# Kernel tuning notes

Measured on AMD Instinct MI355X. Metric: run time of the kernel, lower is better.

The kernel has to match this reference:

```python
import jax, jax.numpy as jnp
import numpy as np


def setup_inputs() -> dict:
    key = jax.random.key(0)
    ks = jax.random.split(key, 6)
    B, U, T, E, H = 8, 128, 256, 128, 128
    # Xavier-uniform scale for linear layers
    def xavier(k, shape):
        fan_in, fan_out = shape[0], shape[1]
        lim = jnp.sqrt(6.0 / (fan_in + fan_out))
        return jax.random.uniform(k, shape, jnp.float32, -lim, lim)
    return {
        "ue": jax.random.normal(ks[0], (B, U, E), jnp.float32),
        "te": jax.random.normal(ks[1], (B, T, E), jnp.float32),
        "ge": jax.random.normal(ks[2], (B, E), jnp.float32),
        "W1": xavier(ks[3], (3 * E, H)),
        "b1": jnp.zeros((H,), jnp.float32),
        "W2": xavier(ks[4], (H, H)),
        "b2": jnp.zeros((H,), jnp.float32),
        "W3": xavier(ks[5], (H, 1)),
        "b3": jnp.zeros((1,), jnp.float32),
    }


def reference(ue, te, ge, W1, b1, W2, b2, W3, b3):
    # Equivalent to cat([u,t,g], -1) @ W1: decompose W1 into per-source blocks
    # and broadcast-add, avoiding the [B,U,T,3E] intermediate.
    E = ue.shape[-1]
    W1u, W1t, W1g = W1[:E], W1[E:2 * E], W1[2 * E:]
    h = (jnp.einsum("bue,eh->buh", ue, W1u)[:, :, None, :]
         + jnp.einsum("bte,eh->bth", te, W1t)[:, None, :, :]
         + (ge @ W1g)[:, None, None, :]
         + b1)                                   # [B,U,T,H]
    h = jax.nn.gelu(h, approximate=False)        # torch nn.GELU default = exact erf
    h = jax.nn.gelu(h @ W2 + b2, approximate=False)
    logits = (h @ W3 + b3)[..., 0]               # [B,U,T]
    B, U, T = logits.shape
    return logits.reshape(B, U * T)
```

## Files before the change

kernel.cpp:

```cpp
#include <hip/hip_runtime.h>
#include <hip/hip_bf16.h>
#include <math.h>

#define E_ 128
#define H_ 128
#define B_ 8
#define U_ 128
#define T_ 256

typedef short short8 __attribute__((ext_vector_type(8)));
typedef unsigned short ushortx8 __attribute__((ext_vector_type(8)));
typedef float floatx4 __attribute__((ext_vector_type(4)));

__device__ __forceinline__ unsigned short f2bf(float f) {
    union { __hip_bfloat16 b; unsigned short u; } cv;
    cv.b = __float2bfloat16(f);
    return cv.u;
}
__device__ __forceinline__ float bf2f(unsigned short u) {
    union { unsigned int u; float f; } cv;
    cv.u = ((unsigned int)u) << 16;
    return cv.f;
}

__device__ __forceinline__ int sw(int row, int cblk) {
    return row * 128 + (((cblk ^ (row & 15)) << 3));
}

__device__ __forceinline__ float gelu_fast(float x) {
    float x2 = x * x;
    float p = x * __builtin_fmaf(x2, 0.1029407583f, 2.3022586210f);
    float e = __builtin_amdgcn_exp2f(-p);
    return x * __builtin_amdgcn_rcpf(1.0f + e);
}

__global__ __launch_bounds__(256) void stage1_kernel(
    const float* __restrict__ ue, const float* __restrict__ te,
    const float* __restrict__ ge, const float* __restrict__ W1,
    const float* __restrict__ b1, const float* __restrict__ W2,
    float* __restrict__ hu_ws, unsigned short* __restrict__ ht_bf,
    float* __restrict__ gu_ws, unsigned short* __restrict__ w2t_ws)
{
    const int blk = blockIdx.x;
    const int tid = threadIdx.x;

    if (blk < 24) {
        __shared__ unsigned short a_s[128 * 128];
        __shared__ unsigned short w_s[128 * 128];
        const float* __restrict__ A;
        const float* __restrict__ W;
        const bool is_ue = (blk < 8);
        if (is_ue) { A = ue + (size_t)blk * 128 * E_;       W = W1; }
        else       { A = te + (size_t)(blk - 8) * 128 * E_; W = W1 + E_ * H_; }

        const float4* __restrict__ Av = (const float4*)A;
        #pragma unroll
        for (int i = 0; i < 16; i++) {
            const int v = tid + i * 256;
            const int row = v >> 5, c4 = (v & 31) * 4;
            const float4 f = Av[v];
            ushort4 u4 = make_ushort4(f2bf(f.x), f2bf(f.y), f2bf(f.z), f2bf(f.w));
            *(ushort4*)(&a_s[sw(row, c4 >> 3) + (c4 & 7)]) = u4;
        }
        const float4* __restrict__ Wv = (const float4*)W;
        #pragma unroll
        for (int i = 0; i < 16; i++) {
            const int v = tid + i * 256;
            const int k = v >> 5, n4 = (v & 31) * 4;
            const float4 f = Wv[v];
            const int c = k >> 3, off = k & 7;
            w_s[sw(n4 + 0, c) + off] = f2bf(f.x);
            w_s[sw(n4 + 1, c) + off] = f2bf(f.y);
            w_s[sw(n4 + 2, c) + off] = f2bf(f.z);
            w_s[sw(n4 + 3, c) + off] = f2bf(f.w);
        }
        __syncthreads();

        const int wave = tid >> 6, lane = tid & 63;
        const int quad = lane >> 4, l16 = lane & 15;
        const int r0 = wave * 32 + l16;

        floatx4 acc[2][8];
        #pragma unroll
        for (int m = 0; m < 2; m++)
            #pragma unroll
            for (int nt = 0; nt < 8; nt++) acc[m][nt] = (floatx4){0.f, 0.f, 0.f, 0.f};

        #pragma unroll
        for (int kk = 0; kk < 4; kk++) {
            const int c = kk * 4 + quad;
            short8 af0 = *(const short8*)(&a_s[sw(r0, c)]);
            short8 af1 = *(const short8*)(&a_s[sw(r0 + 16, c)]);
            #pragma unroll
            for (int nt = 0; nt < 8; nt++) {
                short8 bf = *(const short8*)(&w_s[sw(nt * 16 + l16, c)]);
                acc[0][nt] = __builtin_amdgcn_mfma_f32_16x16x32_bf16(af0, bf, acc[0][nt], 0, 0, 0);
                acc[1][nt] = __builtin_amdgcn_mfma_f32_16x16x32_bf16(af1, bf, acc[1][nt], 0, 0, 0);
            }
        }
        if (is_ue) {
            float* __restrict__ outp = hu_ws + (size_t)blk * 128 * H_;
            #pragma unroll
            for (int m = 0; m < 2; m++) {
                const int rowb = wave * 32 + m * 16 + quad * 4;
                #pragma unroll
                for (int nt = 0; nt < 8; nt++) {
                    const int col = nt * 16 + l16;
                    #pragma unroll
                    for (int r = 0; r < 4; r++)
                        outp[(size_t)(rowb + r) * H_ + col] = acc[m][nt][r];
                }
            }
        } else {
            unsigned short* __restrict__ outp = ht_bf + (size_t)(blk - 8) * 128 * H_;
            #pragma unroll
            for (int m = 0; m < 2; m++) {
                const int rowb = wave * 32 + m * 16 + quad * 4;
                #pragma unroll
                for (int nt = 0; nt < 8; nt++) {
                    const int col = nt * 16 + l16;
                    #pragma unroll
                    for (int r = 0; r < 4; r++)
                        outp[(size_t)(rowb + r) * H_ + col] = f2bf(acc[m][nt][r]);
                }
            }
        }
    } else if (blk < 28) {
        __shared__ float ge_s[2][E_];
        const int rbase = (blk - 24) * 2;
        const int half = tid >> 7, n = tid & 127;
        ge_s[half][n] = ge[(rbase + half) * E_ + n];
        __syncthreads();
        const float* __restrict__ W1g = W1 + 2 * E_ * H_;
        float acc = b1[n];
        #pragma unroll 8
        for (int e = 0; e < E_; e++)
            acc = __builtin_fmaf(ge_s[half][e], W1g[e * H_ + n], acc);
        gu_ws[(rbase + half) * H_ + n] = acc;
    } else {
        const int base = (blk - 28) * 2048;
        #pragma unroll
        for (int i = 0; i < 8; i++) {
            const int o = base + tid + i * 256;
            const int n = o >> 7, k = o & 127;
            w2t_ws[o] = f2bf(W2[k * H_ + n]);
        }
    }
}

__global__ __launch_bounds__(256, 2) void stage2_kernel(
    const float* __restrict__ hu_ws, const unsigned short* __restrict__ ht_bf,
    const float* __restrict__ gu_ws,
    const unsigned short* __restrict__ w2t_ws,
    const float* __restrict__ b2, const float* __restrict__ W3,
    const float* __restrict__ b3, float* __restrict__ out)
{
    __shared__ unsigned short w2s[128 * 128];
    __shared__ unsigned short ht_s[128 * 128];
    __shared__ float hu_s[H_];
    __shared__ float b2_s[H_];
    __shared__ float w3_s[H_];

    const int tid = threadIdx.x;
    const int t0 = blockIdx.x * 128;
    const int u  = blockIdx.y;
    const int b  = blockIdx.z;

    #pragma unroll
    for (int i = 0; i < 8; i++) {
        const int v = tid + i * 256;
        const int n = v >> 4, c = v & 15;
        *(ushortx8*)(&w2s[sw(n, c)]) = *(const ushortx8*)(w2t_ws + n * 128 + c * 8);
    }
    const unsigned short* __restrict__ htg = ht_bf + ((size_t)(b * T_ + t0)) * H_;
    #pragma unroll
    for (int i = 0; i < 8; i++) {
        const int v = tid + i * 256;
        const int row = v >> 4, c = v & 15;
        *(ushortx8*)(&ht_s[sw(row, c)]) = *(const ushortx8*)(htg + row * 128 + c * 8);
    }
    if (tid < H_) {
        hu_s[tid] = hu_ws[((b << 7) + u) * H_ + tid] + gu_ws[b * H_ + tid];
        b2_s[tid] = b2[tid];
        w3_s[tid] = W3[tid];
    }
    __syncthreads();

    const int wave = tid >> 6, lane = tid & 63;
    const int quad = lane >> 4, l16 = lane & 15;
    const int r0 = wave * 32 + l16;

    floatx4 acc[2][8];
    #pragma unroll
    for (int m = 0; m < 2; m++)
        #pragma unroll
        for (int nt = 0; nt < 8; nt++) acc[m][nt] = (floatx4){0.f, 0.f, 0.f, 0.f};

    #pragma unroll
    for (int kk = 0; kk < 4; kk++) {
        const int c = kk * 4 + quad;
        const int k0 = c << 3;
        ushortx8 u0 = *(const ushortx8*)(&ht_s[sw(r0, c)]);
        ushortx8 u1 = *(const ushortx8*)(&ht_s[sw(r0 + 16, c)]);
        const float4 h0 = *(const float4*)(&hu_s[k0]);
        const float4 h1 = *(const float4*)(&hu_s[k0 + 4]);
        const float hv[8] = {h0.x, h0.y, h0.z, h0.w, h1.x, h1.y, h1.z, h1.w};
        short8 af0, af1;
        #pragma unroll
        for (int j = 0; j < 8; j++) {
            af0[j] = (short)f2bf(gelu_fast(bf2f(u0[j]) + hv[j]));
            af1[j] = (short)f2bf(gelu_fast(bf2f(u1[j]) + hv[j]));
        }
        #pragma unroll
        for (int nt = 0; nt < 8; nt++) {
            short8 bf = *(const short8*)(&w2s[sw(nt * 16 + l16, c)]);
            acc[0][nt] = __builtin_amdgcn_mfma_f32_16x16x32_bf16(af0, bf, acc[0][nt], 0, 0, 0);
            acc[1][nt] = __builtin_amdgcn_mfma_f32_16x16x32_bf16(af1, bf, acc[1][nt], 0, 0, 0);
        }
    }

    const float b3v = b3[0];
    float psum[2][4] = {{0.f, 0.f, 0.f, 0.f}, {0.f, 0.f, 0.f, 0.f}};
    #pragma unroll
    for (int nt = 0; nt < 8; nt++) {
        const int n = nt * 16 + l16;
        const float bb = b2_s[n];
        const float ww = w3_s[n];
        #pragma unroll
        for (int m = 0; m < 2; m++)
            #pragma unroll
            for (int r = 0; r < 4; r++)
                psum[m][r] += gelu_fast(acc[m][nt][r] + bb) * ww;
    }
    #pragma unroll
    for (int s = 8; s >= 1; s >>= 1) {
        #pragma unroll
        for (int m = 0; m < 2; m++)
            #pragma unroll
            for (int r = 0; r < 4; r++)
                psum[m][r] += __shfl_xor(psum[m][r], s, 64);
    }
    if (l16 == 0) {
        #pragma unroll
        for (int m = 0; m < 2; m++) {
            const int rowb = t0 + wave * 32 + m * 16 + quad * 4;
            float4 o = make_float4(psum[m][0] + b3v, psum[m][1] + b3v,
                                   psum[m][2] + b3v, psum[m][3] + b3v);
            *(float4*)(out + (size_t)((b << 7) + u) * T_ + rowb) = o;
        }
    }
}

extern "C" void kernel_launch(void* const* d_in, const int* in_sizes, int n_in,
                              void* d_out, int out_size, void* d_ws, size_t ws_size,
                              hipStream_t stream)
{
    const float* ue = (const float*)d_in[0];
    const float* te = (const float*)d_in[1];
    const float* ge = (const float*)d_in[2];
    const float* W1 = (const float*)d_in[3];
    const float* b1 = (const float*)d_in[4];
    const float* W2 = (const float*)d_in[5];
    const float* b2 = (const float*)d_in[6];
    const float* W3 = (const float*)d_in[7];
    const float* b3 = (const float*)d_in[8];
    float* out = (float*)d_out;

    char* ws = (char*)d_ws;
    float* hu_ws = (float*)ws;
    unsigned short* ht_bf = (unsigned short*)(ws + 512 * 1024);
    unsigned short* w2t_ws = (unsigned short*)(ws + 1024 * 1024);
    float* gu_ws = (float*)(ws + 1056 * 1024);

    stage1_kernel<<<dim3(36), dim3(256), 0, stream>>>(
        ue, te, ge, W1, b1, W2, hu_ws, ht_bf, gu_ws, w2t_ws);
    stage2_kernel<<<dim3(T_ / 128, U_, B_), dim3(256), 0, stream>>>(
        hu_ws, ht_bf, gu_ws, w2t_ws, b2, W3, b3, out);
}
```

Measured before the change: 105.2 us.

## Store ht in MFMA fragment order and load it directly into registers

Stage 1 now writes the bf16 te-projection in a layout that matches the MFMA A-fragment order. Stage 2 then reads each lane's fragment straight from global memory with register prefetch of the next k-step, and no longer stages it through shared memory. This cuts stage 2's LDS footprint from 64KB to about 32KB, so launch bounds rise to 4 blocks per CU for more occupancy. The cost is more global/L2 traffic per block, and a register budget tightened by the higher occupancy hint.

```diff
diff --git a/kernel.cpp b/kernel.cpp
--- a/kernel.cpp
+++ b/kernel.cpp
@@ -34,11 +34,12 @@
     return x * __builtin_amdgcn_rcpf(1.0f + e);
 }
 
+
 __global__ __launch_bounds__(256) void stage1_kernel(
     const float* __restrict__ ue, const float* __restrict__ te,
     const float* __restrict__ ge, const float* __restrict__ W1,
     const float* __restrict__ b1, const float* __restrict__ W2,
-    float* __restrict__ hu_ws, unsigned short* __restrict__ ht_bf,
+    float* __restrict__ hu_ws, unsigned short* __restrict__ ht_frag,
     float* __restrict__ gu_ws, unsigned short* __restrict__ w2t_ws)
 {
     const int blk = blockIdx.x;
@@ -112,16 +113,16 @@
                 }
             }
         } else {
-            unsigned short* __restrict__ outp = ht_bf + (size_t)(blk - 8) * 128 * H_;
+            const int tg_base = (blk - 8) * 8 + (tid >> 6) * 2;
             #pragma unroll
             for (int m = 0; m < 2; m++) {
-                const int rowb = wave * 32 + m * 16 + quad * 4;
                 #pragma unroll
                 for (int nt = 0; nt < 8; nt++) {
-                    const int col = nt * 16 + l16;
+                    const size_t base = ((size_t)(tg_base + m) * 16 + nt * 2 + (l16 >> 3)) * 128
+                                      + (l16 & 7);
                     #pragma unroll
                     for (int r = 0; r < 4; r++)
-                        outp[(size_t)(rowb + r) * H_ + col] = f2bf(acc[m][nt][r]);
+                        ht_frag[base + (quad * 4 + r) * 8] = f2bf(acc[m][nt][r]);
                 }
             }
         }
@@ -148,15 +149,14 @@
     }
 }
 
-__global__ __launch_bounds__(256, 2) void stage2_kernel(
-    const float* __restrict__ hu_ws, const unsigned short* __restrict__ ht_bf,
+__global__ __launch_bounds__(256, 4) void stage2_kernel(
+    const float* __restrict__ hu_ws, const unsigned short* __restrict__ ht_frag,
     const float* __restrict__ gu_ws,
     const unsigned short* __restrict__ w2t_ws,
     const float* __restrict__ b2, const float* __restrict__ W3,
     const float* __restrict__ b3, float* __restrict__ out)
 {
     __shared__ unsigned short w2s[128 * 128];
-    __shared__ unsigned short ht_s[128 * 128];
     __shared__ float hu_s[H_];
     __shared__ float b2_s[H_];
     __shared__ float w3_s[H_];
@@ -172,13 +172,6 @@
         const int n = v >> 4, c = v & 15;
         *(ushortx8*)(&w2s[sw(n, c)]) = *(const ushortx8*)(w2t_ws + n * 128 + c * 8);
     }
-    const unsigned short* __restrict__ htg = ht_bf + ((size_t)(b * T_ + t0)) * H_;
-    #pragma unroll
-    for (int i = 0; i < 8; i++) {
-        const int v = tid + i * 256;
-        const int row = v >> 4, c = v & 15;
-        *(ushortx8*)(&ht_s[sw(row, c)]) = *(const ushortx8*)(htg + row * 128 + c * 8);
-    }
     if (tid < H_) {
         hu_s[tid] = hu_ws[((b << 7) + u) * H_ + tid] + gu_ws[b * H_ + tid];
         b2_s[tid] = b2[tid];
@@ -188,7 +181,11 @@
 
     const int wave = tid >> 6, lane = tid & 63;
     const int quad = lane >> 4, l16 = lane & 15;
-    const int r0 = wave * 32 + l16;
+
+    const int tg0 = ((b * T_ + t0) >> 4) + wave * 2;
+    const unsigned short* __restrict__ hp0 =
+        ht_frag + ((size_t)tg0 * 16 + quad) * 128 + l16 * 8;
+    const unsigned short* __restrict__ hp1 = hp0 + 16 * 128;
 
     floatx4 acc[2][8];
     #pragma unroll
@@ -196,27 +193,34 @@
         #pragma unroll
         for (int nt = 0; nt < 8; nt++) acc[m][nt] = (floatx4){0.f, 0.f, 0.f, 0.f};
 
+    ushortx8 c0 = *(const ushortx8*)hp0;
+    ushortx8 c1 = *(const ushortx8*)hp1;
+
     #pragma unroll
     for (int kk = 0; kk < 4; kk++) {
-        const int c = kk * 4 + quad;
-        const int k0 = c << 3;
-        ushortx8 u0 = *(const ushortx8*)(&ht_s[sw(r0, c)]);
-        ushortx8 u1 = *(const ushortx8*)(&ht_s[sw(r0 + 16, c)]);
+        ushortx8 n0, n1;
+        if (kk < 3) {
+            n0 = *(const ushortx8*)(hp0 + (kk + 1) * 512);
+            n1 = *(const ushortx8*)(hp1 + (kk + 1) * 512);
+        }
+        const int k0 = kk * 32 + quad * 8;
         const float4 h0 = *(const float4*)(&hu_s[k0]);
         const float4 h1 = *(const float4*)(&hu_s[k0 + 4]);
         const float hv[8] = {h0.x, h0.y, h0.z, h0.w, h1.x, h1.y, h1.z, h1.w};
         short8 af0, af1;
         #pragma unroll
         for (int j = 0; j < 8; j++) {
-            af0[j] = (short)f2bf(gelu_fast(bf2f(u0[j]) + hv[j]));
-            af1[j] = (short)f2bf(gelu_fast(bf2f(u1[j]) + hv[j]));
-        }
+            af0[j] = (short)f2bf(gelu_fast(bf2f(c0[j]) + hv[j]));
+            af1[j] = (short)f2bf(gelu_fast(bf2f(c1[j]) + hv[j]));
+        }
+        const int c = kk * 4 + quad;
         #pragma unroll
         for (int nt = 0; nt < 8; nt++) {
             short8 bf = *(const short8*)(&w2s[sw(nt * 16 + l16, c)]);
             acc[0][nt] = __builtin_amdgcn_mfma_f32_16x16x32_bf16(af0, bf, acc[0][nt], 0, 0, 0);
             acc[1][nt] = __builtin_amdgcn_mfma_f32_16x16x32_bf16(af1, bf, acc[1][nt], 0, 0, 0);
         }
+        c0 = n0; c1 = n1;
     }
 
     const float b3v = b3[0];
@@ -268,12 +272,12 @@
 
     char* ws = (char*)d_ws;
     float* hu_ws = (float*)ws;
-    unsigned short* ht_bf = (unsigned short*)(ws + 512 * 1024);
+    unsigned short* ht_frag = (unsigned short*)(ws + 512 * 1024);
     unsigned short* w2t_ws = (unsigned short*)(ws + 1024 * 1024);
     float* gu_ws = (float*)(ws + 1056 * 1024);
 
     stage1_kernel<<<dim3(36), dim3(256), 0, stream>>>(
-        ue, te, ge, W1, b1, W2, hu_ws, ht_bf, gu_ws, w2t_ws);
+        ue, te, ge, W1, b1, W2, hu_ws, ht_frag, gu_ws, w2t_ws);
     stage2_kernel<<<dim3(T_ / 128, U_, B_), dim3(256), 0, stream>>>(
-        hu_ws, ht_bf, gu_ws, w2t_ws, b2, W3, b3, out);
-}
+        hu_ws, ht_frag, gu_ws, w2t_ws, b2, W3, b3, out);
+}
```

Measured after the change: 99.16 us. 1.06x faster.
